# Kernel optimization log

Hardware: AMD Instinct MI355X
Metric: run time of the kernel (lower is better)

The kernel has to match this reference:

```python
import jax, jax.numpy as jnp
import numpy as np


def _euclidean_cdist(x, q):
    # torch.cdist with p=2: pairwise L2 distances, shape [B, Q]
    x2 = jnp.sum(x * x, axis=-1, keepdims=True)          # [B, 1]
    q2 = jnp.sum(q * q, axis=-1)[None, :]                # [1, Q]
    d2 = x2 + q2 - 2.0 * (x @ q.T)                        # [B, Q]
    return jnp.sqrt(jnp.maximum(d2, 0.0))


def setup_inputs() -> dict:
    key = jax.random.key(0)
    k1, k2 = jax.random.split(key)
    x = jax.random.normal(k1, (1024, 256), dtype=jnp.float32)
    queue = jax.random.normal(k2, (32768, 256), dtype=jnp.float32)
    return {"x": x, "queue": queue}


def reference(x, queue):
    # Queue update: concat then keep the newest max_size rows (queue assumed full)
    max_size = queue.shape[0]
    q = jnp.concatenate([queue, x], axis=0)[-max_size:]   # [Q, F]
    # Distance matrix + top-2 nearest (topk of negated distances)
    d = _euclidean_cdist(x, q)                            # [B, Q]
    _, idx = jax.lax.top_k(-d, 2)                         # [B, 2]
    # Second-nearest neighbor (first is the point itself, dist 0)
    return q[idx[:, 1]]                                   # [B, F]
```

## Files before the change

### kernel.cpp

```cpp
#include <hip/hip_runtime.h>
#include <stdint.h>

#define B_ROWS 1024
#define FEAT   256
#define QSZ    32768
#define SHIFT  1024
#define QX     (QSZ - B_ROWS)
#define NQB    256
#define MARGIN 8.0f

typedef float v4f __attribute__((ext_vector_type(4)));
typedef short v8s __attribute__((ext_vector_type(8)));

__device__ __forceinline__ uint32_t key_flip(uint32_t u) {
    return u ^ ((uint32_t)((int32_t)u >> 31) | 0x80000000u);
}
__device__ __forceinline__ float key_m(uint32_t k) {
    uint32_t u = k & 0xFFFF8000u;
    u = (u & 0x80000000u) ? (u ^ 0x80000000u) : ~u;
    return __uint_as_float(u);
}
__device__ __forceinline__ void k2_insert(uint32_t& k1, uint32_t& k2, uint32_t key) {
    uint32_t hi = max(k1, key); k1 = min(k1, key); k2 = min(k2, hi);
}
__device__ __forceinline__ uint2 k2_merge(uint2 a, uint2 b) {
    uint32_t hi = max(a.x, b.x);
    uint2 r; r.x = min(a.x, b.x); r.y = min(min(a.y, b.y), hi);
    return r;
}

struct Top2 { float m1; int j1; float m2; int j2; };
__device__ __forceinline__ bool better(float ma, int ja, float mb, int jb) {
    return (ma < mb) || (ma == mb && ja < jb);
}
__device__ __forceinline__ void t2_insert(Top2& t, float m, int j) {
    if (better(m, j, t.m1, t.j1)) { t.m2 = t.m1; t.j2 = t.j1; t.m1 = m; t.j1 = j; }
    else if (better(m, j, t.m2, t.j2)) { t.m2 = m; t.j2 = j; }
}

__device__ __forceinline__ const float* q_row_ptr(int j, const float* x, const float* queue) {
    return (j < QX) ? (queue + (size_t)(j + SHIFT) * FEAT) : (x + (size_t)(j - QX) * FEAT);
}

__device__ __forceinline__ unsigned short f2bf(float f) {
    uint32_t u = __float_as_uint(f);
    uint32_t r = u + 0x7FFFu + ((u >> 16) & 1u);
    return (unsigned short)(r >> 16);
}

__device__ __forceinline__ void lds_load16(const void* g, void* l) {
    __builtin_amdgcn_global_load_lds(
        (const __attribute__((address_space(1))) uint32_t*)g,
        (__attribute__((address_space(3))) uint32_t*)l, 16, 0, 0);
}

__global__ __launch_bounds__(256) void convert_kernel(const float* __restrict__ x,
                                                      const float* __restrict__ queue,
                                                      unsigned short* __restrict__ q_bf,
                                                      float* __restrict__ q2) {
    int wave = threadIdx.x >> 6, lane = threadIdx.x & 63;
    int j = blockIdx.x * 4 + wave;
    const float4* row = (const float4*)q_row_ptr(j, x, queue);
    float4 v = row[lane];
    float s = v.x * v.x + v.y * v.y + v.z * v.z + v.w * v.w;
#pragma unroll
    for (int off = 32; off; off >>= 1) s += __shfl_xor(s, off, 64);
    if (lane == 0) q2[j] = s;
    ushort4 h;
    h.x = f2bf(v.x); h.y = f2bf(v.y); h.z = f2bf(v.z); h.w = f2bf(v.w);
    ((ushort4*)q_bf)[(size_t)j * 64 + lane] = h;
}

__global__ __launch_bounds__(256, 2) void nn_mfma(const unsigned short* __restrict__ q_bf,
                                                  const float* __restrict__ q2,
                                                  uint2* __restrict__ partials) {
    __shared__ unsigned short As0[128 * 64];
    __shared__ unsigned short As1[128 * 64];
    __shared__ unsigned short Bs[128 * 64];
    __shared__ float sq2[256];

    const int t    = threadIdx.x;
    const int w    = t >> 6, lane = t & 63;
    const int wm   = w >> 1, wn = w & 1;
    const int quad = lane >> 4, l16 = lane & 15;

    const int id  = blockIdx.x;
    const int sub = id >> 3;
    const int gx  = sub & 7;
    const int gyU = (id & 7) * 16 + (sub >> 3);

    const unsigned short* x_bf  = q_bf + (size_t)QX * FEAT;
    const unsigned short* aBase = q_bf + (size_t)gyU * 256 * FEAT;
    const unsigned short* bBase = x_bf + (size_t)gx * 128 * FEAT;

    sq2[t] = q2[gyU * 256 + t];

    v4f acc[2][4][4];
#pragma unroll
    for (int h = 0; h < 2; ++h)
#pragma unroll
        for (int a = 0; a < 4; ++a)
#pragma unroll
            for (int b = 0; b < 4; ++b) acc[h][a][b] = (v4f)0.0f;

    const int srow = lane >> 3;
    const int sg   = (lane & 7) ^ srow;

#pragma unroll
    for (int kk = 0; kk < 4; ++kk) {
        int row = w * 32 + kk * 8 + srow;
        int ldsrow = (w * 32 + kk * 8) * 64;
        lds_load16(aBase + (size_t)row * FEAT + sg * 8,         &As0[ldsrow]);
        lds_load16(aBase + (size_t)(row + 128) * FEAT + sg * 8, &As1[ldsrow]);
        lds_load16(bBase + (size_t)row * FEAT + sg * 8,         &Bs[ldsrow]);
    }

    for (int c = 0; c < 4; ++c) {
        __syncthreads();
#pragma unroll
        for (int ks = 0; ks < 2; ++ks) {
            v8s fa0[4], fa1[4], fb[4];
            const int goff  = (((ks * 4 + quad) ^ (l16 & 7)) << 4);
            const int abase = (wm * 64 + l16) * 128 + goff;
            const int bbase = (wn * 64 + l16) * 128 + goff;
#pragma unroll
            for (int tm = 0; tm < 4; ++tm) {
                fa0[tm] = *(const v8s*)((const char*)As0 + abase + tm * 2048);
                fa1[tm] = *(const v8s*)((const char*)As1 + abase + tm * 2048);
            }
#pragma unroll
            for (int tn = 0; tn < 4; ++tn)
                fb[tn] = *(const v8s*)((const char*)Bs + bbase + tn * 2048);
#pragma unroll
            for (int tm = 0; tm < 4; ++tm)
#pragma unroll
                for (int tn = 0; tn < 4; ++tn) {
                    acc[0][tm][tn] = __builtin_amdgcn_mfma_f32_16x16x32_bf16(fa0[tm], fb[tn], acc[0][tm][tn], 0, 0, 0);
                    acc[1][tm][tn] = __builtin_amdgcn_mfma_f32_16x16x32_bf16(fa1[tm], fb[tn], acc[1][tm][tn], 0, 0, 0);
                }
        }
        __syncthreads();
        if (c < 3) {
#pragma unroll
            for (int kk = 0; kk < 4; ++kk) {
                int row = w * 32 + kk * 8 + srow;
                int ldsrow = (w * 32 + kk * 8) * 64;
                lds_load16(aBase + (size_t)row * FEAT + (c + 1) * 64 + sg * 8,         &As0[ldsrow]);
                lds_load16(aBase + (size_t)(row + 128) * FEAT + (c + 1) * 64 + sg * 8, &As1[ldsrow]);
                lds_load16(bBase + (size_t)row * FEAT + (c + 1) * 64 + sg * 8,         &Bs[ldsrow]);
            }
        }
    }

    uint2* scr = (uint2*)As0;
#pragma unroll
    for (int h = 0; h < 2; ++h) {
        float q2r[4][4];
#pragma unroll
        for (int tm = 0; tm < 4; ++tm)
#pragma unroll
            for (int r = 0; r < 4; ++r)
                q2r[tm][r] = sq2[h * 128 + wm * 64 + tm * 16 + quad * 4 + r];
        const int jbase = gyU * 256 + h * 128 + wm * 64 + quad * 4;

#pragma unroll
        for (int tn = 0; tn < 4; ++tn) {
            uint32_t k1 = 0xFFFFFFFFu, k2 = 0xFFFFFFFFu;
#pragma unroll
            for (int tm = 0; tm < 4; ++tm)
#pragma unroll
                for (int r = 0; r < 4; ++r) {
                    float m = fmaf(-2.0f, acc[h][tm][tn][r], q2r[tm][r]);
                    uint32_t u = key_flip(__float_as_uint(m));
                    uint32_t key = (u & 0xFFFF8000u) | (uint32_t)(jbase + tm * 16 + r);
                    k2_insert(k1, k2, key);
                }
#pragma unroll
            for (int mask = 16; mask <= 32; mask <<= 1) {
                uint32_t o1 = __shfl_xor(k1, mask, 64);
                uint32_t o2 = __shfl_xor(k2, mask, 64);
                uint32_t hi = max(k1, o1);
                k1 = min(k1, o1);
                k2 = min(min(k2, o2), hi);
            }
            if (quad == 0)
                scr[(h * 128 + wn * 64 + tn * 16 + l16) * 2 + wm] = make_uint2(k1, k2);
        }
    }
    __syncthreads();
    if (t < 128) {
#pragma unroll
        for (int h = 0; h < 2; ++h) {
            uint2 r = k2_merge(scr[(h * 128 + t) * 2], scr[(h * 128 + t) * 2 + 1]);
            partials[(size_t)(gx * 128 + t) * NQB + (gyU * 2 + h)] = r;
        }
    }
}

__global__ __launch_bounds__(64) void nn_finalize(const float* __restrict__ x,
                                                  const float* __restrict__ queue,
                                                  const float* __restrict__ q2,
                                                  const uint2* __restrict__ partials,
                                                  float* __restrict__ out) {
    __shared__ int list[64];
    __shared__ int s_cnt;

    const int i = blockIdx.x, lane = threadIdx.x;
    if (lane == 0) s_cnt = 0;

    const uint2* p = partials + (size_t)i * NQB;
    uint2 mine[4];
#pragma unroll
    for (int u = 0; u < 4; ++u) mine[u] = p[lane + 64 * u];
    uint2 a = k2_merge(k2_merge(mine[0], mine[1]), k2_merge(mine[2], mine[3]));
#pragma unroll
    for (int mask = 1; mask <= 32; mask <<= 1) {
        uint2 o;
        o.x = __shfl_xor(a.x, mask, 64);
        o.y = __shfl_xor(a.y, mask, 64);
        a = k2_merge(a, o);
    }
    float cutf = key_m(a.y) + MARGIN;
    uint32_t kcut = key_flip(__float_as_uint(cutf)) | 0x7FFFu;

#pragma unroll
    for (int u = 0; u < 4; ++u) {
        if (mine[u].x <= kcut) list[atomicAdd(&s_cnt, 1) & 63] = (int)(mine[u].x & 0x7FFFu);
        if (mine[u].y <= kcut) list[atomicAdd(&s_cnt, 1) & 63] = (int)(mine[u].y & 0x7FFFu);
    }
    __syncthreads();
    int n = min(s_cnt, 64);

    float4 xv = ((const float4*)(x + (size_t)i * FEAT))[lane];
    Top2 bst;
    bst.m1 = __builtin_inff(); bst.j1 = 0x7FFFFFFF;
    bst.m2 = __builtin_inff(); bst.j2 = 0x7FFFFFFF;
    for (int c = 0; c < n; ++c) {
        int j = list[c];
        float4 qv = ((const float4*)q_row_ptr(j, x, queue))[lane];
        float s = qv.x * xv.x + qv.y * xv.y + qv.z * xv.z + qv.w * xv.w;
#pragma unroll
        for (int off = 32; off; off >>= 1) s += __shfl_xor(s, off, 64);
        float m = q2[j] - 2.0f * s;
        t2_insert(bst, m, j);
    }
    int j2 = bst.j2;
    float4 o = ((const float4*)q_row_ptr(j2, x, queue))[lane];
    ((float4*)(out + (size_t)i * FEAT))[lane] = o;
}

extern "C" void kernel_launch(void* const* d_in, const int* in_sizes, int n_in,
                              void* d_out, int out_size, void* d_ws, size_t ws_size,
                              hipStream_t stream) {
    const float* x     = (const float*)d_in[0];
    const float* queue = (const float*)d_in[1];

    unsigned short* q_bf     = (unsigned short*)d_ws;
    float*          q2       = (float*)((char*)d_ws + (16u << 20));
    uint2*          partials = (uint2*)((char*)d_ws + (17u << 20));

    convert_kernel<<<QSZ / 4, 256, 0, stream>>>(x, queue, q_bf, q2);
    nn_mfma<<<1024, 256, 0, stream>>>(q_bf, q2, partials);
    nn_finalize<<<B_ROWS, 64, 0, stream>>>(x, queue, q2, partials, (float*)d_out);
}
```

Before: 115.2 us.

## Restructure MFMA tile: full-K LDS A tile, B fragments held in registers

Each block now handles a 128x128 tile instead of 256x128, so the grid doubles to 2048 blocks. The whole K=256 depth of the queue tile is staged into LDS in one shot, and the x-side fragments are loaded straight from global memory into registers for all K slices. This removes the four-chunk K loop, its repeated barriers and the per-chunk reloads, and q2 is read directly instead of through shared memory. In exchange it uses more registers for the B fragments and a 64KB LDS tile, which may limit occupancy, and the x data is reloaded by twice as many blocks.

```diff
diff --git a/kernel.cpp b/kernel.cpp
--- a/kernel.cpp
+++ b/kernel.cpp
@@ -74,126 +74,105 @@
 __global__ __launch_bounds__(256, 2) void nn_mfma(const unsigned short* __restrict__ q_bf,
                                                   const float* __restrict__ q2,
                                                   uint2* __restrict__ partials) {
-    __shared__ unsigned short As0[128 * 64];
-    __shared__ unsigned short As1[128 * 64];
-    __shared__ unsigned short Bs[128 * 64];
-    __shared__ float sq2[256];
+    __shared__ unsigned short As[128 * 256];
 
     const int t    = threadIdx.x;
     const int w    = t >> 6, lane = t & 63;
     const int wm   = w >> 1, wn = w & 1;
     const int quad = lane >> 4, l16 = lane & 15;
-
-    const int id  = blockIdx.x;
-    const int sub = id >> 3;
-    const int gx  = sub & 7;
-    const int gyU = (id & 7) * 16 + (sub >> 3);
+    const int c3   = l16 & 7;
+
+    const int id = blockIdx.x;
+    const int s_ = id >> 3;
+    const int gy = (id & 7) * 32 + (s_ & 31);
+    const int gx = s_ >> 5;
 
     const unsigned short* x_bf  = q_bf + (size_t)QX * FEAT;
-    const unsigned short* aBase = q_bf + (size_t)gyU * 256 * FEAT;
+    const unsigned short* aBase = q_bf + (size_t)gy * 128 * FEAT;
     const unsigned short* bBase = x_bf + (size_t)gx * 128 * FEAT;
 
-    sq2[t] = q2[gyU * 256 + t];
-
-    v4f acc[2][4][4];
-#pragma unroll
-    for (int h = 0; h < 2; ++h)
-#pragma unroll
-        for (int a = 0; a < 4; ++a)
-#pragma unroll
-            for (int b = 0; b < 4; ++b) acc[h][a][b] = (v4f)0.0f;
-
-    const int srow = lane >> 3;
-    const int sg   = (lane & 7) ^ srow;
-
-#pragma unroll
-    for (int kk = 0; kk < 4; ++kk) {
-        int row = w * 32 + kk * 8 + srow;
-        int ldsrow = (w * 32 + kk * 8) * 64;
-        lds_load16(aBase + (size_t)row * FEAT + sg * 8,         &As0[ldsrow]);
-        lds_load16(aBase + (size_t)(row + 128) * FEAT + sg * 8, &As1[ldsrow]);
-        lds_load16(bBase + (size_t)row * FEAT + sg * 8,         &Bs[ldsrow]);
-    }
-
-    for (int c = 0; c < 4; ++c) {
-        __syncthreads();
-#pragma unroll
-        for (int ks = 0; ks < 2; ++ks) {
-            v8s fa0[4], fa1[4], fb[4];
-            const int goff  = (((ks * 4 + quad) ^ (l16 & 7)) << 4);
-            const int abase = (wm * 64 + l16) * 128 + goff;
-            const int bbase = (wn * 64 + l16) * 128 + goff;
-#pragma unroll
-            for (int tm = 0; tm < 4; ++tm) {
-                fa0[tm] = *(const v8s*)((const char*)As0 + abase + tm * 2048);
-                fa1[tm] = *(const v8s*)((const char*)As1 + abase + tm * 2048);
+    v8s fb[4][8];
+#pragma unroll
+    for (int tn = 0; tn < 4; ++tn) {
+        const unsigned short* brow = bBase + (size_t)(wn * 64 + tn * 16 + l16) * FEAT + quad * 8;
+#pragma unroll
+        for (int ks = 0; ks < 8; ++ks)
+            fb[tn][ks] = *(const v8s*)(brow + ks * 32);
+    }
+
+#pragma unroll
+    for (int i = 0; i < 16; ++i) {
+        int rowp = w * 32 + i * 2;
+        int row  = rowp + (lane >> 5);
+        int g    = (lane & 31) ^ (row & 7);
+        lds_load16(aBase + (size_t)row * FEAT + g * 8, &As[rowp * 256]);
+    }
+
+    v4f acc[4][4];
+#pragma unroll
+    for (int a = 0; a < 4; ++a)
+#pragma unroll
+        for (int b = 0; b < 4; ++b) acc[a][b] = (v4f)0.0f;
+
+    __syncthreads();
+
+#pragma unroll
+    for (int ks = 0; ks < 8; ++ks) {
+        const int gofs = (((ks * 4 + quad) ^ c3) << 4);
+        v8s fa[4];
+#pragma unroll
+        for (int tm = 0; tm < 4; ++tm)
+            fa[tm] = *(const v8s*)((const char*)As + (wm * 64 + tm * 16 + l16) * 512 + gofs);
+#pragma unroll
+        for (int tm = 0; tm < 4; ++tm)
+#pragma unroll
+            for (int tn = 0; tn < 4; ++tn)
+                acc[tm][tn] = __builtin_amdgcn_mfma_f32_16x16x32_bf16(fa[tm], fb[tn][ks], acc[tm][tn], 0, 0, 0);
+    }
+
+    const int jbase = gy * 128 + wm * 64 + quad * 4;
+    float q2r[4][4];
+#pragma unroll
+    for (int tm = 0; tm < 4; ++tm) {
+        v4f qq = *(const v4f*)(q2 + jbase + tm * 16);
+#pragma unroll
+        for (int r = 0; r < 4; ++r) q2r[tm][r] = qq[r];
+    }
+
+    uint2 best[4];
+#pragma unroll
+    for (int tn = 0; tn < 4; ++tn) {
+        uint32_t k1 = 0xFFFFFFFFu, k2 = 0xFFFFFFFFu;
+#pragma unroll
+        for (int tm = 0; tm < 4; ++tm)
+#pragma unroll
+            for (int r = 0; r < 4; ++r) {
+                float m = fmaf(-2.0f, acc[tm][tn][r], q2r[tm][r]);
+                uint32_t u = key_flip(__float_as_uint(m));
+                uint32_t key = (u & 0xFFFF8000u) | (uint32_t)(jbase + tm * 16 + r);
+                k2_insert(k1, k2, key);
             }
 #pragma unroll
-            for (int tn = 0; tn < 4; ++tn)
-                fb[tn] = *(const v8s*)((const char*)Bs + bbase + tn * 2048);
-#pragma unroll
-            for (int tm = 0; tm < 4; ++tm)
-#pragma unroll
-                for (int tn = 0; tn < 4; ++tn) {
-                    acc[0][tm][tn] = __builtin_amdgcn_mfma_f32_16x16x32_bf16(fa0[tm], fb[tn], acc[0][tm][tn], 0, 0, 0);
-                    acc[1][tm][tn] = __builtin_amdgcn_mfma_f32_16x16x32_bf16(fa1[tm], fb[tn], acc[1][tm][tn], 0, 0, 0);
-                }
+        for (int mask = 16; mask <= 32; mask <<= 1) {
+            uint32_t o1 = __shfl_xor(k1, mask, 64);
+            uint32_t o2 = __shfl_xor(k2, mask, 64);
+            uint32_t hi = max(k1, o1);
+            k1 = min(k1, o1);
+            k2 = min(min(k2, o2), hi);
         }
-        __syncthreads();
-        if (c < 3) {
-#pragma unroll
-            for (int kk = 0; kk < 4; ++kk) {
-                int row = w * 32 + kk * 8 + srow;
-                int ldsrow = (w * 32 + kk * 8) * 64;
-                lds_load16(aBase + (size_t)row * FEAT + (c + 1) * 64 + sg * 8,         &As0[ldsrow]);
-                lds_load16(aBase + (size_t)(row + 128) * FEAT + (c + 1) * 64 + sg * 8, &As1[ldsrow]);
-                lds_load16(bBase + (size_t)row * FEAT + (c + 1) * 64 + sg * 8,         &Bs[ldsrow]);
-            }
-        }
-    }
-
-    uint2* scr = (uint2*)As0;
-#pragma unroll
-    for (int h = 0; h < 2; ++h) {
-        float q2r[4][4];
-#pragma unroll
-        for (int tm = 0; tm < 4; ++tm)
-#pragma unroll
-            for (int r = 0; r < 4; ++r)
-                q2r[tm][r] = sq2[h * 128 + wm * 64 + tm * 16 + quad * 4 + r];
-        const int jbase = gyU * 256 + h * 128 + wm * 64 + quad * 4;
-
-#pragma unroll
-        for (int tn = 0; tn < 4; ++tn) {
-            uint32_t k1 = 0xFFFFFFFFu, k2 = 0xFFFFFFFFu;
-#pragma unroll
-            for (int tm = 0; tm < 4; ++tm)
-#pragma unroll
-                for (int r = 0; r < 4; ++r) {
-                    float m = fmaf(-2.0f, acc[h][tm][tn][r], q2r[tm][r]);
-                    uint32_t u = key_flip(__float_as_uint(m));
-                    uint32_t key = (u & 0xFFFF8000u) | (uint32_t)(jbase + tm * 16 + r);
-                    k2_insert(k1, k2, key);
-                }
-#pragma unroll
-            for (int mask = 16; mask <= 32; mask <<= 1) {
-                uint32_t o1 = __shfl_xor(k1, mask, 64);
-                uint32_t o2 = __shfl_xor(k2, mask, 64);
-                uint32_t hi = max(k1, o1);
-                k1 = min(k1, o1);
-                k2 = min(min(k2, o2), hi);
-            }
-            if (quad == 0)
-                scr[(h * 128 + wn * 64 + tn * 16 + l16) * 2 + wm] = make_uint2(k1, k2);
-        }
+        best[tn] = make_uint2(k1, k2);
+    }
+    __syncthreads();
+    uint2* scr = (uint2*)As;
+    if (quad == 0) {
+#pragma unroll
+        for (int tn = 0; tn < 4; ++tn)
+            scr[(wn * 64 + tn * 16 + l16) * 2 + wm] = best[tn];
     }
     __syncthreads();
     if (t < 128) {
-#pragma unroll
-        for (int h = 0; h < 2; ++h) {
-            uint2 r = k2_merge(scr[(h * 128 + t) * 2], scr[(h * 128 + t) * 2 + 1]);
-            partials[(size_t)(gx * 128 + t) * NQB + (gyU * 2 + h)] = r;
-        }
+        uint2 r = k2_merge(scr[t * 2], scr[t * 2 + 1]);
+        partials[(size_t)(gx * 128 + t) * NQB + gy] = r;
     }
 }
 
@@ -260,6 +239,6 @@
     uint2*          partials = (uint2*)((char*)d_ws + (17u << 20));
 
     convert_kernel<<<QSZ / 4, 256, 0, stream>>>(x, queue, q_bf, q2);
-    nn_mfma<<<1024, 256, 0, stream>>>(q_bf, q2, partials);
+    nn_mfma<<<2048, 256, 0, stream>>>(q_bf, q2, partials);
     nn_finalize<<<B_ROWS, 64, 0, stream>>>(x, queue, q2, partials, (float*)d_out);
 }
```

Result: slower. 134.1 us (+16.4%).
